# Optimization experiments

Measured on AMD Instinct MI355X. Metric: run time of the kernel, lower is better.

Reference implementation:

```python
import jax, jax.numpy as jnp
import numpy as np

F = 256   # nb_features
H = 8     # nb_heads
B = 4
S = 1024  # q_s == kv_s
SCALE = F ** 0.5  # module MULTIPLIES scores by sqrt(f) when scale=True


def setup_inputs() -> dict:
    key = jax.random.key(0)
    ks = jax.random.split(key, 6)
    return {
        "q_input": jax.random.normal(ks[0], (B, F, S), dtype=jnp.float32),
        "kv_input": jax.random.normal(ks[1], (B, F, S), dtype=jnp.float32),
        "Wq": jax.random.normal(ks[2], (F, F * H), dtype=jnp.float32) * (F ** -0.5),
        "Wk": jax.random.normal(ks[3], (F, F * H), dtype=jnp.float32) * (F ** -0.5),
        "Wv": jax.random.normal(ks[4], (F, F * H), dtype=jnp.float32) * (F ** -0.5),
        "Wz": jax.random.normal(ks[5], (F * H, F), dtype=jnp.float32) * ((F * H) ** -0.5),
    }


def reference(q_input, kv_input, Wq, Wk, Wv, Wz):
    b, f, q_s = q_input.shape
    kv_s = kv_input.shape[2]
    h = H
    # (b, f, s) -> (b, s, f)
    qx = jnp.transpose(q_input, (0, 2, 1))
    kvx = jnp.transpose(kv_input, (0, 2, 1))
    # Linear f -> f*h, then split last dim into (f, h)
    q = (qx @ Wq).reshape(b, q_s, f, h)
    k = (kvx @ Wk).reshape(b, kv_s, f, h)
    v = (kvx @ Wv).reshape(b, kv_s, f, h)
    # sigmoid-gated attention: scores MULTIPLIED by sqrt(f)
    qkt = jnp.einsum('bifh,bjfh->bijh', q, k)
    attn = jax.nn.sigmoid(qkt * SCALE)
    weighted_v = jnp.einsum('bijh,bjfh->bifh', attn, v)  # (b, q_s, f, h)
    z = weighted_v.reshape(b * q_s, f * h)
    out = jax.nn.relu(z @ Wz)  # dropout p=0.0 -> identity
    return jnp.transpose(out.reshape(b, q_s, f), (0, 2, 1))  # (b, f, q_s)
```

## Files before the change

kernel.cpp:

```cpp
#include <hip/hip_runtime.h>
#include <hip/hip_fp16.h>

typedef _Float16 f16;
typedef _Float16 f16x8 __attribute__((ext_vector_type(8)));
typedef float f32x4 __attribute__((ext_vector_type(4)));
typedef unsigned u32x4 __attribute__((ext_vector_type(4)));

#define AS1(p) ((const __attribute__((address_space(1))) void*)(p))
#define AS3(p) ((__attribute__((address_space(3))) void*)(p))

__device__ __forceinline__ void gload16(const void* g, void* l) {
  __builtin_amdgcn_global_load_lds(AS1(g), AS3(l), 16, 0, 0);
}

__device__ __forceinline__ float sgm(float x) {
  return __builtin_amdgcn_rcpf(1.0f + __builtin_amdgcn_exp2f(x * -23.083120654223414f));
}

__device__ __forceinline__ void tbody(const float* __restrict__ ip,
                                      f16* __restrict__ op,
                                      long in_rs, long out_rs) {
  __shared__ float t[64][68];
  int tid = threadIdx.x;
  {
    int c4 = (tid & 15) * 4, r0 = tid >> 4;
#pragma unroll
    for (int p = 0; p < 4; ++p) {
      int r = r0 + 16 * p;
      float4 v = *(const float4*)(ip + (long)r * in_rs + c4);
      t[c4 + 0][r] = v.x; t[c4 + 1][r] = v.y; t[c4 + 2][r] = v.z; t[c4 + 3][r] = v.w;
    }
  }
  __syncthreads();
  {
    int r4 = (tid & 15) * 4, c0 = tid >> 4;
#pragma unroll
    for (int p = 0; p < 4; ++p) {
      int c = c0 + 16 * p;
      float4 v = *(const float4*)(&t[c][r4]);
      union { f16 h[4]; unsigned long long u; } pk;
      pk.h[0] = (f16)v.x; pk.h[1] = (f16)v.y; pk.h[2] = (f16)v.z; pk.h[3] = (f16)v.w;
      *(unsigned long long*)(op + (long)c * out_rs + r4) = pk.u;
    }
  }
}

__global__ __launch_bounds__(256) void tall(
    const float* __restrict__ qin, const float* __restrict__ kvin,
    const float* __restrict__ Wq, const float* __restrict__ Wk,
    const float* __restrict__ Wv, const float* __restrict__ Wz,
    f16* __restrict__ Xq, f16* __restrict__ Xkv,
    f16* __restrict__ Wqt, f16* __restrict__ Wkt, f16* __restrict__ Wvt,
    f16* __restrict__ Wzt) {
  int id = blockIdx.x;
  if (id < 512) {
    int x = id & 15, y = (id >> 4) & 3, z = id >> 6;
    const float* in = (z < 4) ? qin : kvin;
    f16* out = (z < 4) ? Xq : Xkv;
    long b = z & 3;
    tbody(in + b * 262144 + (long)(y * 64) * 1024 + x * 64,
          out + b * 262144 + (long)(x * 64) * 256 + y * 64, 1024, 256);
  } else if (id < 896) {
    int t = id - 512;
    int x = t & 31, y = (t >> 5) & 3, z = t >> 7;
    const float* in = (z == 0) ? Wq : (z == 1) ? Wk : Wv;
    f16* out = (z == 0) ? Wqt : (z == 1) ? Wkt : Wvt;
    tbody(in + (long)(y * 64) * 2048 + x * 64,
          out + (long)(x * 64) * 256 + y * 64, 2048, 256);
  } else {
    int t = id - 896;
    int x = t & 3, y = (t >> 2) & 3;
    long z = t >> 4;
    tbody(Wz + z * 256 + (long)(y * 64) * 2048 + x * 64,
          Wzt + z * 256 + (long)(x * 64) * 2048 + y * 64, 2048, 2048);
  }
}

__global__ __launch_bounds__(256) void projk(
    const f16* __restrict__ Xq, const f16* __restrict__ Xkv,
    const f16* __restrict__ Wqt, const f16* __restrict__ Wkt, const f16* __restrict__ Wvt,
    f16* __restrict__ Qh, f16* __restrict__ Kh, f16* __restrict__ Vt) {
  __shared__ char sm[65536];
  int z = blockIdx.z;
  const f16* A = (z == 0) ? Xq : Xkv;
  const f16* B = (z == 0) ? Wqt : (z == 1) ? Wkt : Wvt;
  int m0 = blockIdx.x * 128, n0 = blockIdx.y * 128;
  int tid = threadIdx.x, wave = tid >> 6, lane = tid & 63;
  int wm = wave & 1, wn = wave >> 1;
  f32x4 acc[4][4];
#pragma unroll
  for (int i = 0; i < 4; ++i)
#pragma unroll
    for (int j = 0; j < 4; ++j) acc[i][j] = (f32x4){0.f, 0.f, 0.f, 0.f};

  auto PSTAGE = [&](int buf, int kt) {
    char* As = sm + buf * 32768;
    char* Bs = As + 16384;
    int k0 = kt * 64;
#pragma unroll
    for (int is = 0; is < 4; ++is) {
      int loff = is * 4096 + wave * 1024;
      int g = loff + lane * 16;
      int row = g >> 7, sl = (g >> 4) & 7;
      int sp = (sl ^ (row & 7)) * 8;
      gload16(A + (long)(m0 + row) * 256 + k0 + sp, As + loff);
      gload16(B + (long)(n0 + row) * 256 + k0 + sp, Bs + loff);
    }
  };

  PSTAGE(0, 0);
  __syncthreads();
  for (int kt = 0; kt < 4; ++kt) {
    int cur = kt & 1;
    if (kt < 3) PSTAGE(cur ^ 1, kt + 1);
    const char* As = sm + cur * 32768;
    const char* Bs = As + 16384;
#pragma unroll
    for (int t = 0; t < 2; ++t) {
      f16x8 af[4], bf[4];
#pragma unroll
      for (int mi = 0; mi < 4; ++mi) {
        int row = wm * 64 + mi * 16 + (lane & 15);
        int sl = (t * 4 + (lane >> 4)) ^ (row & 7);
        af[mi] = *(const f16x8*)(As + row * 128 + sl * 16);
      }
#pragma unroll
      for (int ni = 0; ni < 4; ++ni) {
        int row = wn * 64 + ni * 16 + (lane & 15);
        int sl = (t * 4 + (lane >> 4)) ^ (row & 7);
        bf[ni] = *(const f16x8*)(Bs + row * 128 + sl * 16);
      }
#pragma unroll
      for (int mi = 0; mi < 4; ++mi)
#pragma unroll
        for (int ni = 0; ni < 4; ++ni)
          acc[mi][ni] = __builtin_amdgcn_mfma_f32_16x16x32_f16(af[mi], bf[ni], acc[mi][ni], 0, 0, 0);
    }
    __syncthreads();
  }
#pragma unroll
  for (int mi = 0; mi < 4; ++mi)
#pragma unroll
    for (int ni = 0; ni < 4; ++ni) {
      int cc = wn * 64 + ni * 16 + (lane & 15);
      int rs0 = wm * 64 + mi * 16 + (lane >> 4) * 4;
      union { f16 h[4]; unsigned long long u; } pk;
#pragma unroll
      for (int r = 0; r < 4; ++r) pk.h[r] = (f16)acc[mi][ni][r];
      *(unsigned long long*)(sm + cc * 272 + rs0 * 2) = pk.u;
    }
  __syncthreads();
  if (z < 2) {
    f16* outp = (z == 0) ? Qh : Kh;
#pragma unroll
    for (int pass = 0; pass < 4; ++pass) {
      int item = pass * 256 + tid;
      int rs = item & 127, h = item >> 7;
      int m = m0 + rs, b = m >> 10, s = m & 1023;
      union { unsigned short u16[16]; uint4 q[2]; } pk;
#pragma unroll
      for (int u = 0; u < 16; ++u)
        pk.u16[u] = *(const unsigned short*)(sm + (h + 8 * u) * 272 + rs * 2);
      f16* dst = outp + ((long)(b * 8 + h) * 1024 + s) * 256 + (n0 >> 3);
      *(uint4*)dst = pk.q[0];
      *(uint4*)(dst + 8) = pk.q[1];
    }
  } else {
    int cc = tid >> 1, half = tid & 1;
    int c = n0 + cc, h = c & 7, fi = c >> 3;
    int m = m0 + half * 64;
    int b = m >> 10, s0 = m & 1023;
    uint4 q[8];
#pragma unroll
    for (int j = 0; j < 8; ++j)
      q[j] = *(const uint4*)(sm + cc * 272 + half * 128 + j * 16);
    f16* dst = Vt + ((long)(b * 8 + h) * 256 + fi) * 1024 + s0;
#pragma unroll
    for (int j = 0; j < 8; ++j) *(uint4*)(dst + j * 8) = q[j];
  }
}

__global__ __launch_bounds__(256) void attnk(
    const f16* __restrict__ Qh, const f16* __restrict__ Kh,
    const f16* __restrict__ Vt, f16* __restrict__ Zb) {
  __shared__ char sm[65536];
  int flat = blockIdx.x;
  int xcd = flat & 7, slotb = flat >> 3;
  int bh = xcd + 8 * (slotb & 3);
  int i0 = (slotb >> 2) * 64;
  int tid = threadIdx.x, wave = tid >> 6, lane = tid & 63;
  int l15 = lane & 15, l4 = lane >> 4;
  const f16* Qp = Qh + (long)bh * 262144;
  f16x8 q[8];
  {
    const f16* qr = Qp + (long)(i0 + wave * 16 + l15) * 256 + l4 * 8;
#pragma unroll
    for (int t = 0; t < 8; ++t) q[t] = *(const f16x8*)(qr + t * 32);
  }
  f32x4 acc[16];
#pragma unroll
  for (int n = 0; n < 16; ++n) acc[n] = (f32x4){0.f, 0.f, 0.f, 0.f};

  const char* kp[4];
  const char* vp[4];
  {
    const char* Kb = (const char*)(Kh + (long)bh * 262144);
    const char* Vb = (const char*)(Vt + (long)bh * 262144);
#pragma unroll
    for (int is = 0; is < 4; ++is) {
      int g = is * 4096 + wave * 1024 + lane * 16;
      int krow = g >> 9, ksl = (g >> 4) & 31;
      kp[is] = Kb + krow * 512 + ((ksl ^ krow) * 16);
      int f = g >> 6, jc = (g >> 4) & 3;
      vp[is] = Vb + f * 2048 + ((jc ^ ((f >> 1) & 3)) * 16);
    }
  }
  const int KB  = l15 * 512 + ((l4 * 16) ^ (l15 * 16));
  const int KB2 = KB + 8448;
  const int VB  = 16384 + l15 * 64 + ((l4 ^ ((l15 >> 1) & 3)) * 16);
  const int sdo = wave * 1024;

  auto STAGE = [&](int ob) {
#pragma unroll
    for (int is = 0; is < 4; ++is) {
      gload16(kp[is], sm + ob + is * 4096 + sdo);
      gload16(vp[is], sm + ob + 16384 + is * 4096 + sdo);
      kp[is] += 16384;
      vp[is] += 64;
    }
  };

  STAGE(0);
  STAGE(32768);
  int bb = 0;
  for (int jt = 0; jt < 32; ++jt) {
    if (jt < 31) asm volatile("s_waitcnt vmcnt(8)" ::: "memory");
    else         asm volatile("s_waitcnt vmcnt(0)" ::: "memory");
    __builtin_amdgcn_s_barrier();
    __builtin_amdgcn_sched_barrier(0);
    const int kb = KB ^ bb, kb2 = KB2 ^ bb, vb = VB ^ bb;
    f32x4 s0 = (f32x4){0.f, 0.f, 0.f, 0.f};
    f32x4 s1 = (f32x4){0.f, 0.f, 0.f, 0.f};
    __builtin_amdgcn_s_setprio(1);
#pragma unroll
    for (int t = 0; t < 8; ++t) {
      f16x8 k0 = *(const f16x8*)(sm + (kb ^ (t * 64)));
      f16x8 k1 = *(const f16x8*)(sm + (kb2 ^ (t * 64)));
      s0 = __builtin_amdgcn_mfma_f32_16x16x32_f16(k0, q[t], s0, 0, 0, 0);
      s1 = __builtin_amdgcn_mfma_f32_16x16x32_f16(k1, q[t], s1, 0, 0, 0);
    }
    __builtin_amdgcn_s_setprio(0);
    unsigned u00 = __builtin_bit_cast(unsigned, __builtin_amdgcn_cvt_pkrtz(sgm(s0[0]), sgm(s0[1])));
    unsigned u01 = __builtin_bit_cast(unsigned, __builtin_amdgcn_cvt_pkrtz(sgm(s0[2]), sgm(s0[3])));
    unsigned u10 = __builtin_bit_cast(unsigned, __builtin_amdgcn_cvt_pkrtz(sgm(s1[0]), sgm(s1[1])));
    unsigned u11 = __builtin_bit_cast(unsigned, __builtin_amdgcn_cvt_pkrtz(sgm(s1[2]), sgm(s1[3])));
    auto a0 = __builtin_amdgcn_permlane32_swap(u00, u10, false, false);
    auto w02 = __builtin_amdgcn_permlane16_swap(a0[0], a0[1], false, false);
    auto a1 = __builtin_amdgcn_permlane32_swap(u01, u11, false, false);
    auto w13 = __builtin_amdgcn_permlane16_swap(a1[0], a1[1], false, false);
    u32x4 paw;
    paw[0] = w02[0]; paw[1] = w13[0]; paw[2] = w02[1]; paw[3] = w13[1];
    f16x8 pav = __builtin_bit_cast(f16x8, paw);
    __builtin_amdgcn_s_setprio(1);
#pragma unroll
    for (int n = 0; n < 16; ++n) {
      f16x8 vbf = *(const f16x8*)(sm + (vb ^ (n * 1024)));
      acc[n] = __builtin_amdgcn_mfma_f32_16x16x32_f16(pav, vbf, acc[n], 0, 0, 0);
    }
    __builtin_amdgcn_s_setprio(0);
    __builtin_amdgcn_sched_barrier(0);
    asm volatile("s_waitcnt lgkmcnt(0)" ::: "memory");
    __builtin_amdgcn_s_barrier();
    __builtin_amdgcn_sched_barrier(0);
    if (jt < 30) STAGE(bb);
    bb ^= 32768;
  }
#pragma unroll
  for (int nf = 0; nf < 16; ++nf)
#pragma unroll
    for (int r = 0; r < 4; ++r) {
      int il = wave * 16 + l4 * 4 + r;
      int f = nf * 16 + l15;
      *(f16*)(sm + il * 512 + ((f * 2) ^ (((il >> 2) & 3) << 5))) = (f16)acc[nf][r];
    }
  __syncthreads();
  f16* zp = Zb + ((long)bh * 1024 + i0) * 256;
#pragma unroll
  for (int c = 0; c < 8; ++c) {
    int il = c * 8 + (tid >> 5);
    int fb = (tid & 31) * 16;
    uint4 v = *(const uint4*)(sm + il * 512 + (fb ^ (((il >> 2) & 3) << 5)));
    *(uint4*)((char*)zp + il * 512 + fb) = v;
  }
}

__global__ __launch_bounds__(256) void zkern(
    const f16* __restrict__ Wzt, const f16* __restrict__ Zb,
    float* __restrict__ out) {
  __shared__ char sm[65536];
  int fo0 = blockIdx.x * 64, s0 = blockIdx.y * 64, b = blockIdx.z;
  int tid = threadIdx.x, wave = tid >> 6, lane = tid & 63;
  int wm = wave & 1, wn = wave >> 1;
  f32x4 acc[2][2];
#pragma unroll
  for (int i = 0; i < 2; ++i)
#pragma unroll
    for (int j = 0; j < 2; ++j) acc[i][j] = (f32x4){0.f, 0.f, 0.f, 0.f};

  auto ZSTAGE = [&](int buf, int kt) {
    char* As = sm + buf * 32768;
    char* Bs = As + 16384;
    int k0 = kt * 128, h = k0 >> 8, fi0 = k0 & 255;
#pragma unroll
    for (int is = 0; is < 4; ++is) {
      int loff = is * 4096 + wave * 1024;
      int g = loff + lane * 16;
      int row = g >> 8, sl = (g >> 4) & 15;
      int sp = (sl ^ (row & 15)) * 8;
      gload16(Wzt + (long)(fo0 + row) * 2048 + k0 + sp, As + loff);
      gload16(Zb + ((long)(b * 8 + h) * 1024 + s0 + row) * 256 + fi0 + sp, Bs + loff);
    }
  };

  ZSTAGE(0, 0);
  __syncthreads();
  for (int kt = 0; kt < 16; ++kt) {
    int cur = kt & 1;
    if (kt < 15) ZSTAGE(cur ^ 1, kt + 1);
    const char* As = sm + cur * 32768;
    const char* Bs = As + 16384;
#pragma unroll
    for (int t = 0; t < 4; ++t) {
      f16x8 af[2], bf[2];
#pragma unroll
      for (int mi = 0; mi < 2; ++mi) {
        int row = wm * 32 + mi * 16 + (lane & 15);
        int sl = (t * 4 + (lane >> 4)) ^ (row & 15);
        af[mi] = *(const f16x8*)(As + row * 256 + sl * 16);
      }
#pragma unroll
      for (int ni = 0; ni < 2; ++ni) {
        int row = wn * 32 + ni * 16 + (lane & 15);
        int sl = (t * 4 + (lane >> 4)) ^ (row & 15);
        bf[ni] = *(const f16x8*)(Bs + row * 256 + sl * 16);
      }
#pragma unroll
      for (int mi = 0; mi < 2; ++mi)
#pragma unroll
        for (int ni = 0; ni < 2; ++ni)
          acc[mi][ni] = __builtin_amdgcn_mfma_f32_16x16x32_f16(af[mi], bf[ni], acc[mi][ni], 0, 0, 0);
    }
    __syncthreads();
  }
#pragma unroll
  for (int mi = 0; mi < 2; ++mi)
#pragma unroll
    for (int ni = 0; ni < 2; ++ni)
#pragma unroll
      for (int r = 0; r < 4; ++r) {
        int fo = fo0 + wm * 32 + mi * 16 + (lane >> 4) * 4 + r;
        int s = s0 + wn * 32 + ni * 16 + (lane & 15);
        float v = acc[mi][ni][r];
        out[((long)b * 256 + fo) * 1024 + s] = v > 0.f ? v : 0.f;
      }
}

extern "C" void kernel_launch(void* const* d_in, const int* in_sizes, int n_in,
                              void* d_out, int out_size, void* d_ws, size_t ws_size,
                              hipStream_t stream) {
  const float* qin = (const float*)d_in[0];
  const float* kvin = (const float*)d_in[1];
  const float* Wq = (const float*)d_in[2];
  const float* Wk = (const float*)d_in[3];
  const float* Wv = (const float*)d_in[4];
  const float* Wz = (const float*)d_in[5];
  float* out = (float*)d_out;
  char* ws = (char*)d_ws;
  const long MB = 1 << 20;
  f16* Xq  = (f16*)(ws + 0 * MB);
  f16* Xkv = (f16*)(ws + 2 * MB);
  f16* Wqt = (f16*)(ws + 4 * MB);
  f16* Wkt = (f16*)(ws + 5 * MB);
  f16* Wvt = (f16*)(ws + 6 * MB);
  f16* Wzt = (f16*)(ws + 7 * MB);
  f16* Qh  = (f16*)(ws + 8 * MB);
  f16* Kh  = (f16*)(ws + 24 * MB);
  f16* Vt  = (f16*)(ws + 40 * MB);
  f16* Zb  = Qh;
  dim3 blk(256);
  tall<<<dim3(1024), blk, 0, stream>>>(qin, kvin, Wq, Wk, Wv, Wz,
                                       Xq, Xkv, Wqt, Wkt, Wvt, Wzt);
  projk<<<dim3(32, 16, 3), blk, 0, stream>>>(Xq, Xkv, Wqt, Wkt, Wvt, Qh, Kh, Vt);
  attnk<<<dim3(512), blk, 0, stream>>>(Qh, Kh, Vt, Zb);
  zkern<<<dim3(4, 16, 4), blk, 0, stream>>>(Wzt, Zb, out);
}
```

Baseline: 113.4 us.

## Process two 16-row query tiles per wave in attention kernel

Each wave now handles 32 query rows instead of 16, so each block covers 128 rows and the grid halves to 256 blocks. Every K and V fragment read from LDS feeds two MFMAs, halving LDS and global K/V traffic per unit of work. The cost is double the accumulator and Q registers, which may lower occupancy or cause spills. 256 blocks also leaves fewer blocks than the MI355X's CUs, so some units may sit idle. The epilogue staging in LDS now fills the full 64 KB buffer.

```diff
diff --git a/kernel.cpp b/kernel.cpp
--- a/kernel.cpp
+++ b/kernel.cpp
@@ -187,19 +187,25 @@
   int flat = blockIdx.x;
   int xcd = flat & 7, slotb = flat >> 3;
   int bh = xcd + 8 * (slotb & 3);
-  int i0 = (slotb >> 2) * 64;
+  int i0 = (slotb >> 2) * 128;
   int tid = threadIdx.x, wave = tid >> 6, lane = tid & 63;
   int l15 = lane & 15, l4 = lane >> 4;
   const f16* Qp = Qh + (long)bh * 262144;
-  f16x8 q[8];
+  f16x8 qA[8], qB[8];
   {
-    const f16* qr = Qp + (long)(i0 + wave * 16 + l15) * 256 + l4 * 8;
-#pragma unroll
-    for (int t = 0; t < 8; ++t) q[t] = *(const f16x8*)(qr + t * 32);
-  }
-  f32x4 acc[16];
-#pragma unroll
-  for (int n = 0; n < 16; ++n) acc[n] = (f32x4){0.f, 0.f, 0.f, 0.f};
+    const f16* qrA = Qp + (long)(i0 + wave * 32 + l15) * 256 + l4 * 8;
+    const f16* qrB = qrA + 16 * 256;
+#pragma unroll
+    for (int t = 0; t < 8; ++t) qA[t] = *(const f16x8*)(qrA + t * 32);
+#pragma unroll
+    for (int t = 0; t < 8; ++t) qB[t] = *(const f16x8*)(qrB + t * 32);
+  }
+  f32x4 accA[16], accB[16];
+#pragma unroll
+  for (int n = 0; n < 16; ++n) {
+    accA[n] = (f32x4){0.f, 0.f, 0.f, 0.f};
+    accB[n] = (f32x4){0.f, 0.f, 0.f, 0.f};
+  }
 
   const char* kp[4];
   const char* vp[4];
@@ -239,33 +245,54 @@
     __builtin_amdgcn_s_barrier();
     __builtin_amdgcn_sched_barrier(0);
     const int kb = KB ^ bb, kb2 = KB2 ^ bb, vb = VB ^ bb;
-    f32x4 s0 = (f32x4){0.f, 0.f, 0.f, 0.f};
-    f32x4 s1 = (f32x4){0.f, 0.f, 0.f, 0.f};
+    f32x4 sA0 = (f32x4){0.f, 0.f, 0.f, 0.f};
+    f32x4 sA1 = (f32x4){0.f, 0.f, 0.f, 0.f};
+    f32x4 sB0 = (f32x4){0.f, 0.f, 0.f, 0.f};
+    f32x4 sB1 = (f32x4){0.f, 0.f, 0.f, 0.f};
     __builtin_amdgcn_s_setprio(1);
 #pragma unroll
     for (int t = 0; t < 8; ++t) {
       f16x8 k0 = *(const f16x8*)(sm + (kb ^ (t * 64)));
       f16x8 k1 = *(const f16x8*)(sm + (kb2 ^ (t * 64)));
-      s0 = __builtin_amdgcn_mfma_f32_16x16x32_f16(k0, q[t], s0, 0, 0, 0);
-      s1 = __builtin_amdgcn_mfma_f32_16x16x32_f16(k1, q[t], s1, 0, 0, 0);
+      sA0 = __builtin_amdgcn_mfma_f32_16x16x32_f16(k0, qA[t], sA0, 0, 0, 0);
+      sB0 = __builtin_amdgcn_mfma_f32_16x16x32_f16(k0, qB[t], sB0, 0, 0, 0);
+      sA1 = __builtin_amdgcn_mfma_f32_16x16x32_f16(k1, qA[t], sA1, 0, 0, 0);
+      sB1 = __builtin_amdgcn_mfma_f32_16x16x32_f16(k1, qB[t], sB1, 0, 0, 0);
     }
     __builtin_amdgcn_s_setprio(0);
-    unsigned u00 = __builtin_bit_cast(unsigned, __builtin_amdgcn_cvt_pkrtz(sgm(s0[0]), sgm(s0[1])));
-    unsigned u01 = __builtin_bit_cast(unsigned, __builtin_amdgcn_cvt_pkrtz(sgm(s0[2]), sgm(s0[3])));
-    unsigned u10 = __builtin_bit_cast(unsigned, __builtin_amdgcn_cvt_pkrtz(sgm(s1[0]), sgm(s1[1])));
-    unsigned u11 = __builtin_bit_cast(unsigned, __builtin_amdgcn_cvt_pkrtz(sgm(s1[2]), sgm(s1[3])));
-    auto a0 = __builtin_amdgcn_permlane32_swap(u00, u10, false, false);
-    auto w02 = __builtin_amdgcn_permlane16_swap(a0[0], a0[1], false, false);
-    auto a1 = __builtin_amdgcn_permlane32_swap(u01, u11, false, false);
-    auto w13 = __builtin_amdgcn_permlane16_swap(a1[0], a1[1], false, false);
-    u32x4 paw;
-    paw[0] = w02[0]; paw[1] = w13[0]; paw[2] = w02[1]; paw[3] = w13[1];
-    f16x8 pav = __builtin_bit_cast(f16x8, paw);
+    f16x8 pavA, pavB;
+    {
+      unsigned u00 = __builtin_bit_cast(unsigned, __builtin_amdgcn_cvt_pkrtz(sgm(sA0[0]), sgm(sA0[1])));
+      unsigned u01 = __builtin_bit_cast(unsigned, __builtin_amdgcn_cvt_pkrtz(sgm(sA0[2]), sgm(sA0[3])));
+      unsigned u10 = __builtin_bit_cast(unsigned, __builtin_amdgcn_cvt_pkrtz(sgm(sA1[0]), sgm(sA1[1])));
+      unsigned u11 = __builtin_bit_cast(unsigned, __builtin_amdgcn_cvt_pkrtz(sgm(sA1[2]), sgm(sA1[3])));
+      auto a0 = __builtin_amdgcn_permlane32_swap(u00, u10, false, false);
+      auto w02 = __builtin_amdgcn_permlane16_swap(a0[0], a0[1], false, false);
+      auto a1 = __builtin_amdgcn_permlane32_swap(u01, u11, false, false);
+      auto w13 = __builtin_amdgcn_permlane16_swap(a1[0], a1[1], false, false);
+      u32x4 paw;
+      paw[0] = w02[0]; paw[1] = w13[0]; paw[2] = w02[1]; paw[3] = w13[1];
+      pavA = __builtin_bit_cast(f16x8, paw);
+    }
+    {
+      unsigned u00 = __builtin_bit_cast(unsigned, __builtin_amdgcn_cvt_pkrtz(sgm(sB0[0]), sgm(sB0[1])));
+      unsigned u01 = __builtin_bit_cast(unsigned, __builtin_amdgcn_cvt_pkrtz(sgm(sB0[2]), sgm(sB0[3])));
+      unsigned u10 = __builtin_bit_cast(unsigned, __builtin_amdgcn_cvt_pkrtz(sgm(sB1[0]), sgm(sB1[1])));
+      unsigned u11 = __builtin_bit_cast(unsigned, __builtin_amdgcn_cvt_pkrtz(sgm(sB1[2]), sgm(sB1[3])));
+      auto a0 = __builtin_amdgcn_permlane32_swap(u00, u10, false, false);
+      auto w02 = __builtin_amdgcn_permlane16_swap(a0[0], a0[1], false, false);
+      auto a1 = __builtin_amdgcn_permlane32_swap(u01, u11, false, false);
+      auto w13 = __builtin_amdgcn_permlane16_swap(a1[0], a1[1], false, false);
+      u32x4 paw;
+      paw[0] = w02[0]; paw[1] = w13[0]; paw[2] = w02[1]; paw[3] = w13[1];
+      pavB = __builtin_bit_cast(f16x8, paw);
+    }
     __builtin_amdgcn_s_setprio(1);
 #pragma unroll
     for (int n = 0; n < 16; ++n) {
       f16x8 vbf = *(const f16x8*)(sm + (vb ^ (n * 1024)));
-      acc[n] = __builtin_amdgcn_mfma_f32_16x16x32_f16(pav, vbf, acc[n], 0, 0, 0);
+      accA[n] = __builtin_amdgcn_mfma_f32_16x16x32_f16(pavA, vbf, accA[n], 0, 0, 0);
+      accB[n] = __builtin_amdgcn_mfma_f32_16x16x32_f16(pavB, vbf, accB[n], 0, 0, 0);
     }
     __builtin_amdgcn_s_setprio(0);
     __builtin_amdgcn_sched_barrier(0);
@@ -279,14 +306,16 @@
   for (int nf = 0; nf < 16; ++nf)
 #pragma unroll
     for (int r = 0; r < 4; ++r) {
-      int il = wave * 16 + l4 * 4 + r;
+      int ilA = wave * 32 + l4 * 4 + r;
+      int ilB = ilA + 16;
       int f = nf * 16 + l15;
-      *(f16*)(sm + il * 512 + ((f * 2) ^ (((il >> 2) & 3) << 5))) = (f16)acc[nf][r];
+      *(f16*)(sm + ilA * 512 + ((f * 2) ^ (((ilA >> 2) & 3) << 5))) = (f16)accA[nf][r];
+      *(f16*)(sm + ilB * 512 + ((f * 2) ^ (((ilB >> 2) & 3) << 5))) = (f16)accB[nf][r];
     }
   __syncthreads();
   f16* zp = Zb + ((long)bh * 1024 + i0) * 256;
 #pragma unroll
-  for (int c = 0; c < 8; ++c) {
+  for (int c = 0; c < 16; ++c) {
     int il = c * 8 + (tid >> 5);
     int fb = (tid & 31) * 16;
     uint4 v = *(const uint4*)(sm + il * 512 + (fb ^ (((il >> 2) & 3) << 5)));
@@ -391,6 +420,6 @@
   tall<<<dim3(1024), blk, 0, stream>>>(qin, kvin, Wq, Wk, Wv, Wz,
                                        Xq, Xkv, Wqt, Wkt, Wvt, Wzt);
   projk<<<dim3(32, 16, 3), blk, 0, stream>>>(Xq, Xkv, Wqt, Wkt, Wvt, Qh, Kh, Vt);
-  attnk<<<dim3(512), blk, 0, stream>>>(Qh, Kh, Vt, Zb);
+  attnk<<<dim3(256), blk, 0, stream>>>(Qh, Kh, Vt, Zb);
   zkern<<<dim3(4, 16, 4), blk, 0, stream>>>(Wzt, Zb, out);
 }
```

After: 123.7 us. 9.2% more time.
